# Kernel tuning notes

Measured on AMD Instinct MI355X. Metric: run time of the kernel, lower is better.

The kernel has to match this reference:

```python
import jax, jax.numpy as jnp
import numpy as np

TOP_K = 2
LB_COEF = 0.01


def setup_inputs() -> dict:
    key = jax.random.key(0)
    k1, k2 = jax.random.split(key)
    x = jax.random.normal(k1, (4, 8192, 2048), dtype=jnp.float32)
    # router weight, torch Linear layout [num_experts, d_model]
    W = jax.random.normal(k2, (64, 2048), dtype=jnp.float32) * (1.0 / np.sqrt(2048))
    return {"x": x, "W": W}


def reference(x, W):
    # logits: [B, S, E]
    logits = jnp.einsum('bsd,ed->bse', x, W)
    top_k_logits, top_k_indices = jax.lax.top_k(logits, TOP_K)
    top_k_probs = jax.nn.softmax(top_k_logits, axis=-1)
    router_probs = jax.nn.softmax(logits, axis=-1)
    expert_probs = router_probs.mean(axis=(0, 1))  # [E]
    lb_loss = LB_COEF * jnp.sum(expert_probs * jnp.log(expert_probs + 1e-8))
    return top_k_probs, top_k_indices, lb_loss
```

## Files before the change

### kernel.cpp

```cpp
#include <hip/hip_runtime.h>

#define BM 64
#define KC 64
#define DD 2048
#define EE 64
#define NROWS 32768

__global__ __launch_bounds__(256) void router_main(const float* __restrict__ x,
                                                   const float* __restrict__ W,
                                                   float* __restrict__ out,
                                                   float* __restrict__ accum) {
    __shared__ float xs[KC][BM];
    __shared__ float ws[KC][EE];
    __shared__ float lg[BM][EE + 1];
    __shared__ float rowinv[BM];

    const int t = threadIdx.x;
    const int row0 = blockIdx.x * BM;

    const int tr = t & 15;
    const int tc = t >> 4;

    const int lrow = t >> 2;
    const int lk4  = (t & 3) * 4;

    float acc[4][4];
#pragma unroll
    for (int i = 0; i < 4; ++i)
#pragma unroll
        for (int j = 0; j < 4; ++j) acc[i][j] = 0.f;

    for (int kb = 0; kb < DD; kb += KC) {
#pragma unroll
        for (int c = 0; c < 4; ++c) {
            const int k = lk4 + c * 16;
            const float4 v = *reinterpret_cast<const float4*>(
                &x[(size_t)(row0 + lrow) * DD + kb + k]);
            xs[k + 0][lrow] = v.x;
            xs[k + 1][lrow] = v.y;
            xs[k + 2][lrow] = v.z;
            xs[k + 3][lrow] = v.w;
        }
#pragma unroll
        for (int c = 0; c < 4; ++c) {
            const int k = lk4 + c * 16;
            const float4 v = *reinterpret_cast<const float4*>(
                &W[(size_t)lrow * DD + kb + k]);
            ws[k + 0][lrow] = v.x;
            ws[k + 1][lrow] = v.y;
            ws[k + 2][lrow] = v.z;
            ws[k + 3][lrow] = v.w;
        }
        __syncthreads();

#pragma unroll
        for (int k = 0; k < KC; ++k) {
            const float4 xa = *reinterpret_cast<const float4*>(&xs[k][tr * 4]);
            const float4 wv = *reinterpret_cast<const float4*>(&ws[k][tc * 4]);
            acc[0][0] = fmaf(xa.x, wv.x, acc[0][0]);
            acc[0][1] = fmaf(xa.x, wv.y, acc[0][1]);
            acc[0][2] = fmaf(xa.x, wv.z, acc[0][2]);
            acc[0][3] = fmaf(xa.x, wv.w, acc[0][3]);
            acc[1][0] = fmaf(xa.y, wv.x, acc[1][0]);
            acc[1][1] = fmaf(xa.y, wv.y, acc[1][1]);
            acc[1][2] = fmaf(xa.y, wv.z, acc[1][2]);
            acc[1][3] = fmaf(xa.y, wv.w, acc[1][3]);
            acc[2][0] = fmaf(xa.z, wv.x, acc[2][0]);
            acc[2][1] = fmaf(xa.z, wv.y, acc[2][1]);
            acc[2][2] = fmaf(xa.z, wv.z, acc[2][2]);
            acc[2][3] = fmaf(xa.z, wv.w, acc[2][3]);
            acc[3][0] = fmaf(xa.w, wv.x, acc[3][0]);
            acc[3][1] = fmaf(xa.w, wv.y, acc[3][1]);
            acc[3][2] = fmaf(xa.w, wv.z, acc[3][2]);
            acc[3][3] = fmaf(xa.w, wv.w, acc[3][3]);
        }
        __syncthreads();
    }

#pragma unroll
    for (int i = 0; i < 4; ++i)
#pragma unroll
        for (int j = 0; j < 4; ++j) lg[tr * 4 + i][tc * 4 + j] = acc[i][j];
    __syncthreads();

    if (t < BM) {
        const int r = t;
        float m1 = -1e30f, m2 = -1e30f;
        int i1 = 0, i2 = 0;
        for (int e = 0; e < EE; ++e) {
            const float l = lg[r][e];
            if (l > m1) {
                m2 = m1; i2 = i1;
                m1 = l;  i1 = e;
            } else if (l > m2) {
                m2 = l; i2 = e;
            }
        }
        float s = 0.f;
        for (int e = 0; e < EE; ++e) {
            const float p = __expf(lg[r][e] - m1);
            lg[r][e] = p;
            s += p;
        }
        rowinv[r] = 1.f / s;

        const float e2  = __expf(m2 - m1);
        const float inv = 1.f / (1.f + e2);
        const size_t gr = (size_t)row0 + r;
        out[2 * gr]     = inv;
        out[2 * gr + 1] = e2 * inv;
        out[2 * (size_t)NROWS + 2 * gr]     = (float)i1;
        out[2 * (size_t)NROWS + 2 * gr + 1] = (float)i2;
    }
    __syncthreads();

    if (t < EE) {
        const int e = t;
        float cs = 0.f;
        for (int r = 0; r < BM; ++r) cs += lg[r][e] * rowinv[r];
        atomicAdd(&accum[e], cs);
    }
}

__global__ void router_loss(const float* __restrict__ accum, float* __restrict__ out) {
    const int e = threadIdx.x;
    const float p = accum[e] * (1.0f / (float)NROWS);
    float v = p * __logf(p + 1e-8f);
#pragma unroll
    for (int off = 32; off > 0; off >>= 1) v += __shfl_down(v, off);
    if (e == 0) out[4 * (size_t)NROWS] = 0.01f * v;
}

extern "C" void kernel_launch(void* const* d_in, const int* in_sizes, int n_in,
                              void* d_out, int out_size, void* d_ws, size_t ws_size,
                              hipStream_t stream) {
    const float* x = (const float*)d_in[0];
    const float* W = (const float*)d_in[1];
    float* out = (float*)d_out;
    float* accum = (float*)d_ws;

    hipMemsetAsync(d_ws, 0, EE * sizeof(float), stream);
    router_main<<<NROWS / BM, 256, 0, stream>>>(x, W, out, accum);
    router_loss<<<1, 64, 0, stream>>>(accum, out);
}
```

Measured before the change: 422.6 us.

## Double-buffer tiles via direct global-to-LDS loads with XOR swizzle and parallel epilogue

Replaces the register-staged transposed shared-memory loads with global_load_lds direct copies into a double-buffered, XOR-swizzled row-major layout, so the load of the next K tile overlaps compute on the current one. The inner loop now reads float4 along K for both operands. The epilogue's top-2 search, softmax and column sums are split across all four wavefronts instead of one, then merged. This uses more LDS (64 KB) and may reduce occupancy.

```diff
diff --git a/kernel.cpp b/kernel.cpp
--- a/kernel.cpp
+++ b/kernel.cpp
@@ -5,121 +5,172 @@
 #define DD 2048
 #define EE 64
 #define NROWS 32768
+#define NTILES (DD / KC)
 
 __global__ __launch_bounds__(256) void router_main(const float* __restrict__ x,
                                                    const float* __restrict__ W,
                                                    float* __restrict__ out,
                                                    float* __restrict__ accum) {
-    __shared__ float xs[KC][BM];
-    __shared__ float ws[KC][EE];
-    __shared__ float lg[BM][EE + 1];
-    __shared__ float rowinv[BM];
+    __shared__ __align__(16) float smem[16384];
 
     const int t = threadIdx.x;
+    const int l = t & 63;
+    const int w = t >> 6;
     const int row0 = blockIdx.x * BM;
+
+    const char* xc = (const char*)x;
+    const char* wc = (const char*)W;
+
+    unsigned gxb[4], gwb[4];
+    int ldsb[4];
+#pragma unroll
+    for (int i = 0; i < 4; ++i) {
+        const int row = i * 16 + w * 4 + (l >> 4);
+        const int c   = (l & 15) ^ ((4 * i + w) & 15);
+        gxb[i]  = (unsigned)((( (unsigned)(row0 + row) * DD ) + c * 4) * 4);
+        gwb[i]  = (unsigned)((( (unsigned)row * DD ) + c * 4) * 4);
+        ldsb[i] = i * 1024 + w * 256;
+    }
+
+#define STAGE(buf, tile) do {                                                          \
+    const unsigned kof_ = (unsigned)(tile) * (KC * 4);                                 \
+    float* bx_ = smem + (buf) * 8192;                                                  \
+    float* bw_ = bx_ + 4096;                                                           \
+    _Pragma("unroll")                                                                  \
+    for (int i_ = 0; i_ < 4; ++i_) {                                                   \
+        __builtin_amdgcn_global_load_lds(                                              \
+            (const __attribute__((address_space(1))) void*)(xc + gxb[i_] + kof_),      \
+            (__attribute__((address_space(3))) void*)(bx_ + ldsb[i_]), 16, 0, 0);      \
+        __builtin_amdgcn_global_load_lds(                                              \
+            (const __attribute__((address_space(1))) void*)(wc + gwb[i_] + kof_),      \
+            (__attribute__((address_space(3))) void*)(bw_ + ldsb[i_]), 16, 0, 0);      \
+    }                                                                                  \
+} while (0)
 
     const int tr = t & 15;
     const int tc = t >> 4;
+    const int trm = tr << 2;
+    const int tcm = tc << 2;
 
-    const int lrow = t >> 2;
-    const int lk4  = (t & 3) * 4;
+    float acc[4][4] = {};
 
-    float acc[4][4];
+    int cur = 0;
+    STAGE(0, 0);
+    __syncthreads();
+
+    for (int tile = 0; tile < NTILES; ++tile) {
+        if (tile + 1 < NTILES) STAGE(cur ^ 1, tile + 1);
+
+        const float* bx = smem + cur * 8192;
+        const float* bw = bx + 4096;
 #pragma unroll
-    for (int i = 0; i < 4; ++i)
+        for (int k4 = 0; k4 < 16; ++k4) {
+            const int xo = trm ^ (k4 << 2);
+            const int wo = tcm ^ (k4 << 2);
+            float4 xa[4], wv[4];
 #pragma unroll
-        for (int j = 0; j < 4; ++j) acc[i][j] = 0.f;
-
-    for (int kb = 0; kb < DD; kb += KC) {
+            for (int i = 0; i < 4; ++i)
+                xa[i] = *reinterpret_cast<const float4*>(bx + ((4 * tr + i) << 6) + xo);
 #pragma unroll
-        for (int c = 0; c < 4; ++c) {
-            const int k = lk4 + c * 16;
-            const float4 v = *reinterpret_cast<const float4*>(
-                &x[(size_t)(row0 + lrow) * DD + kb + k]);
-            xs[k + 0][lrow] = v.x;
-            xs[k + 1][lrow] = v.y;
-            xs[k + 2][lrow] = v.z;
-            xs[k + 3][lrow] = v.w;
-        }
+            for (int j = 0; j < 4; ++j)
+                wv[j] = *reinterpret_cast<const float4*>(bw + ((4 * tc + j) << 6) + wo);
 #pragma unroll
-        for (int c = 0; c < 4; ++c) {
-            const int k = lk4 + c * 16;
-            const float4 v = *reinterpret_cast<const float4*>(
-                &W[(size_t)lrow * DD + kb + k]);
-            ws[k + 0][lrow] = v.x;
-            ws[k + 1][lrow] = v.y;
-            ws[k + 2][lrow] = v.z;
-            ws[k + 3][lrow] = v.w;
+            for (int i = 0; i < 4; ++i)
+#pragma unroll
+                for (int j = 0; j < 4; ++j) {
+                    acc[i][j] = fmaf(xa[i].x, wv[j].x, acc[i][j]);
+                    acc[i][j] = fmaf(xa[i].y, wv[j].y, acc[i][j]);
+                    acc[i][j] = fmaf(xa[i].z, wv[j].z, acc[i][j]);
+                    acc[i][j] = fmaf(xa[i].w, wv[j].w, acc[i][j]);
+                }
         }
         __syncthreads();
+        cur ^= 1;
+    }
 
-#pragma unroll
-        for (int k = 0; k < KC; ++k) {
-            const float4 xa = *reinterpret_cast<const float4*>(&xs[k][tr * 4]);
-            const float4 wv = *reinterpret_cast<const float4*>(&ws[k][tc * 4]);
-            acc[0][0] = fmaf(xa.x, wv.x, acc[0][0]);
-            acc[0][1] = fmaf(xa.x, wv.y, acc[0][1]);
-            acc[0][2] = fmaf(xa.x, wv.z, acc[0][2]);
-            acc[0][3] = fmaf(xa.x, wv.w, acc[0][3]);
-            acc[1][0] = fmaf(xa.y, wv.x, acc[1][0]);
-            acc[1][1] = fmaf(xa.y, wv.y, acc[1][1]);
-            acc[1][2] = fmaf(xa.y, wv.z, acc[1][2]);
-            acc[1][3] = fmaf(xa.y, wv.w, acc[1][3]);
-            acc[2][0] = fmaf(xa.z, wv.x, acc[2][0]);
-            acc[2][1] = fmaf(xa.z, wv.y, acc[2][1]);
-            acc[2][2] = fmaf(xa.z, wv.z, acc[2][2]);
-            acc[2][3] = fmaf(xa.z, wv.w, acc[2][3]);
-            acc[3][0] = fmaf(xa.w, wv.x, acc[3][0]);
-            acc[3][1] = fmaf(xa.w, wv.y, acc[3][1]);
-            acc[3][2] = fmaf(xa.w, wv.z, acc[3][2]);
-            acc[3][3] = fmaf(xa.w, wv.w, acc[3][3]);
-        }
-        __syncthreads();
-    }
+    float* lg     = smem;
+    float* pm1    = smem + 4160;
+    float* pi1    = smem + 4416;
+    float* pm2    = smem + 4672;
+    float* pi2    = smem + 4928;
+    float* rowm   = smem + 5184;
+    float* ps     = smem + 5248;
+    float* rowinv = smem + 5504;
+    float* cpart  = smem + 5568;
 
 #pragma unroll
     for (int i = 0; i < 4; ++i)
 #pragma unroll
-        for (int j = 0; j < 4; ++j) lg[tr * 4 + i][tc * 4 + j] = acc[i][j];
+        for (int j = 0; j < 4; ++j)
+            lg[(4 * tr + i) * 65 + 4 * tc + j] = acc[i][j];
     __syncthreads();
 
-    if (t < BM) {
+    {
+        const int q = t >> 6, r = t & 63;
+        float m1 = -INFINITY, m2 = -INFINITY, i1 = 0.f, i2 = 0.f;
+        const float* rowp = lg + r * 65 + q * 16;
+        for (int e = 0; e < 16; ++e) {
+            const float v = rowp[e];
+            if (v > m1)      { m2 = m1; i2 = i1; m1 = v; i1 = (float)(q * 16 + e); }
+            else if (v > m2) { m2 = v; i2 = (float)(q * 16 + e); }
+        }
+        pm1[q * 64 + r] = m1; pi1[q * 64 + r] = i1;
+        pm2[q * 64 + r] = m2; pi2[q * 64 + r] = i2;
+    }
+    __syncthreads();
+
+    if (t < 64) {
         const int r = t;
-        float m1 = -1e30f, m2 = -1e30f;
-        int i1 = 0, i2 = 0;
-        for (int e = 0; e < EE; ++e) {
-            const float l = lg[r][e];
-            if (l > m1) {
-                m2 = m1; i2 = i1;
-                m1 = l;  i1 = e;
-            } else if (l > m2) {
-                m2 = l; i2 = e;
-            }
+        float m1 = pm1[r], m2 = pm2[r], i1 = pi1[r], i2 = pi2[r];
+        for (int q = 1; q < 4; ++q) {
+            const float b1 = pm1[q * 64 + r], b2 = pm2[q * 64 + r];
+            const float bi1 = pi1[q * 64 + r], bi2 = pi2[q * 64 + r];
+            if (b1 > m1) {
+                if (m1 >= b2) { m2 = m1; i2 = i1; }
+                else          { m2 = b2; i2 = bi2; }
+                m1 = b1; i1 = bi1;
+            } else if (b1 > m2) { m2 = b1; i2 = bi1; }
         }
-        float s = 0.f;
-        for (int e = 0; e < EE; ++e) {
-            const float p = __expf(lg[r][e] - m1);
-            lg[r][e] = p;
-            s += p;
-        }
-        rowinv[r] = 1.f / s;
-
+        rowm[r] = m1;
         const float e2  = __expf(m2 - m1);
-        const float inv = 1.f / (1.f + e2);
+        const float inv = 1.0f / (1.0f + e2);
         const size_t gr = (size_t)row0 + r;
         out[2 * gr]     = inv;
         out[2 * gr + 1] = e2 * inv;
-        out[2 * (size_t)NROWS + 2 * gr]     = (float)i1;
-        out[2 * (size_t)NROWS + 2 * gr + 1] = (float)i2;
+        out[2 * (size_t)NROWS + 2 * gr]     = i1;
+        out[2 * (size_t)NROWS + 2 * gr + 1] = i2;
     }
     __syncthreads();
 
-    if (t < EE) {
-        const int e = t;
+    {
+        const int q = t >> 6, r = t & 63;
+        const float m = rowm[r];
+        float s = 0.f;
+        float* rowp = lg + r * 65 + q * 16;
+        for (int e = 0; e < 16; ++e) {
+            const float p = __expf(rowp[e] - m);
+            rowp[e] = p;
+            s += p;
+        }
+        ps[q * 64 + r] = s;
+    }
+    __syncthreads();
+
+    if (t < 64) rowinv[t] = 1.0f / (ps[t] + ps[64 + t] + ps[128 + t] + ps[192 + t]);
+    __syncthreads();
+
+    {
+        const int e = t & 63, q = t >> 6;
         float cs = 0.f;
-        for (int r = 0; r < BM; ++r) cs += lg[r][e] * rowinv[r];
-        atomicAdd(&accum[e], cs);
+        for (int rr = q * 16; rr < q * 16 + 16; ++rr)
+            cs += lg[rr * 65 + e] * rowinv[rr];
+        cpart[q * 64 + e] = cs;
     }
+    __syncthreads();
+
+    if (t < 64)
+        atomicAdd(&accum[t], cpart[t] + cpart[64 + t] + cpart[128 + t] + cpart[192 + t]);
+#undef STAGE
 }
 
 __global__ void router_loss(const float* __restrict__ accum, float* __restrict__ out) {
```

Result: no change. 423.4 us (+0.2%).
